# Kernel optimization log

Measured on AMD Instinct MI355X. Metric: run time of the kernel, lower is better.

Reference implementation:

```python
import jax, jax.numpy as jnp
import numpy as np

N_NODES = 50000
IN_FT = 64
OUT_FT = 64
J = 3
MAX_SCALE = 2 ** (J - 1)  # 4
TOTAL_DIM = IN_FT * (1 + (J - 1) + J * (J - 1) // 2)  # 6*IN_FT = 384
N_EDGES = 800000


def setup_inputs() -> dict:
    key = jax.random.key(0)
    k1, k2, k3, k4, k5 = jax.random.split(key, 5)
    seq = jax.random.normal(k1, (N_NODES, IN_FT), dtype=jnp.float32)
    edge_index = jax.random.randint(k2, (2, N_EDGES), 0, N_NODES, dtype=jnp.int32)
    edge_weight = jax.random.uniform(k3, (N_EDGES,), dtype=jnp.float32)
    # xavier_normal_ with gain=1.414 on fc.weight [OUT_FT, TOTAL_DIM]
    std = 1.414 * np.sqrt(2.0 / (OUT_FT + TOTAL_DIM))
    fc_w = jax.random.normal(k4, (OUT_FT, TOTAL_DIM), dtype=jnp.float32) * std
    bias = jnp.zeros((OUT_FT,), dtype=jnp.float32)
    prelu_a = jnp.array(0.25, dtype=jnp.float32)  # nn.PReLU default single param
    return {"seq": seq, "edge_index": edge_index, "edge_weight": edge_weight,
            "fc_w": fc_w, "bias": bias, "prelu_a": prelu_a}


def reference(seq, edge_index, edge_weight, fc_w, bias, prelu_a):
    n = seq.shape[0]
    f = seq.shape[1]
    src, dst = edge_index[0], edge_index[1]

    def spmm(x):  # gather source features, scale by edge weight, scatter-add to dest
        return jax.ops.segment_sum(x[src] * edge_weight[:, None], dst, num_segments=n)

    diff_list = []
    x_curr = seq
    for step in range(1, MAX_SCALE + 1):
        x_curr = spmm(x_curr)
        if step & (step - 1) == 0:
            diff_list.append(x_curr)

    F0 = diff_list[-1]
    F1 = jnp.concatenate([jnp.abs(diff_list[i - 1] - diff_list[i])
                          for i in range(1, len(diff_list))], axis=1)

    # second-order features: diffuse concatenated U, take abs diffs of blocks
    U = jnp.concatenate(diff_list, axis=1)  # [N, J*f]
    U_diff = [U]
    for _ in range(1, MAX_SCALE):
        U_diff.append(spmm(U_diff[-1]))
    feats2 = []
    for j in range(J):
        for jp in range(j + 1, J):
            s, e = j * f, (j + 1) * f
            feats2.append(jnp.abs(U_diff[jp][:, s:e] - U_diff[jp - 1][:, s:e]))
    F2 = jnp.concatenate(feats2, axis=1)

    feats = jnp.concatenate([F0, F1, F2], axis=1)  # [N, 6*f]
    out = feats @ fc_w.T + bias
    return jnp.where(out > 0, out, prelu_a * out)
```

## Files before the change

### kernel.cpp

```cpp
#include <hip/hip_runtime.h>
#include <hip/hip_bf16.h>

typedef short short8 __attribute__((ext_vector_type(8)));
typedef float f32x4 __attribute__((ext_vector_type(4)));

static constexpr int F = 64;
static constexpr int TOT = 384;
static constexpr int SLOT = 64;
static constexpr int CAP = 1536;
static constexpr int EPB = 4096;
static constexpr int WPN = 20480;

__device__ __forceinline__ unsigned short f2bf(float f) {
    unsigned u = __builtin_bit_cast(unsigned, f);
    u += 0x7fffu + ((u >> 16) & 1u);
    return (unsigned short)(u >> 16);
}
__device__ __forceinline__ float bflo(unsigned u) {
    return __builtin_bit_cast(float, u << 16);
}
__device__ __forceinline__ float bfhi(unsigned u) {
    return __builtin_bit_cast(float, u & 0xffff0000u);
}


__global__ __launch_bounds__(256) void combo_kernel(
    const float* __restrict__ x, unsigned* __restrict__ xb,
    const float* __restrict__ fcw, unsigned short* __restrict__ wp,
    int* __restrict__ gcur, long long total8, int cvtblocks, int nbuck)
{
    int b = blockIdx.x;
    if (b < cvtblocks) {
        long long i = (long long)b * 256 + threadIdx.x;
        if (i >= total8) return;
        const float4 f0 = *(const float4*)(x + i * 8);
        const float4 f1 = *(const float4*)(x + i * 8 + 4);
        uint4 o;
        o.x = (unsigned)f2bf(f0.x) | ((unsigned)f2bf(f0.y) << 16);
        o.y = (unsigned)f2bf(f0.z) | ((unsigned)f2bf(f0.w) << 16);
        o.z = (unsigned)f2bf(f1.x) | ((unsigned)f2bf(f1.y) << 16);
        o.w = (unsigned)f2bf(f1.z) | ((unsigned)f2bf(f1.w) << 16);
        *(uint4*)(xb + i * 4) = o;
    } else if (b == cvtblocks) {
        for (int e = threadIdx.x; e < WPN; e += 256) {
            int j = e & 7;
            int l = (e >> 3) & 63;
            int t = (e >> 9) & 3;
            int s = e >> 11;
            int k  = s * 32 + ((l >> 4) << 3) + j;
            int nn = t * 16 + (l & 15);
            int c  = k & 63;
            float v;
            if (k < 64)       v = fcw[nn * TOT + c];
            else if (k < 128) v = fcw[nn * TOT + 64 + c] + fcw[nn * TOT + 192 + c];
            else if (k < 192) v = fcw[nn * TOT + 128 + c];
            else if (k < 256) v = fcw[nn * TOT + 256 + c];
            else              v = fcw[nn * TOT + 320 + c];
            wp[e] = f2bf(v);
        }
    } else {
        for (int i = threadIdx.x; i < nbuck; i += 256) gcur[i] = 0;
    }
}


__global__ __launch_bounds__(256) void scatter_bucket(
    const int* __restrict__ src, const int* __restrict__ dst,
    const float* __restrict__ ew, int* __restrict__ gcur,
    int2* __restrict__ ebuf, int ne)
{
    __shared__ int hist[1024];
    __shared__ int base[1024];
    for (int i = threadIdx.x; i < 1024; i += 256) hist[i] = 0;
    __syncthreads();

    long long b0 = (long long)blockIdx.x * EPB;
    int sv[16]; int dv[16]; float wv[16];
#pragma unroll
    for (int j = 0; j < 4; ++j) {
        long long i = b0 + (long long)(threadIdx.x + 256 * j) * 4;
        if (i + 3 < ne) {
            int4   s = *(const int4*)(src + i);
            int4   d = *(const int4*)(dst + i);
            float4 w = *(const float4*)(ew + i);
            sv[j*4+0]=s.x; sv[j*4+1]=s.y; sv[j*4+2]=s.z; sv[j*4+3]=s.w;
            dv[j*4+0]=d.x; dv[j*4+1]=d.y; dv[j*4+2]=d.z; dv[j*4+3]=d.w;
            wv[j*4+0]=w.x; wv[j*4+1]=w.y; wv[j*4+2]=w.z; wv[j*4+3]=w.w;
        } else {
#pragma unroll
            for (int c = 0; c < 4; ++c) {
                long long e = i + c;
                if (e < ne) { sv[j*4+c]=src[e]; dv[j*4+c]=dst[e]; wv[j*4+c]=ew[e]; }
                else dv[j*4+c] = -1;
            }
        }
    }
#pragma unroll
    for (int c = 0; c < 16; ++c)
        if (dv[c] >= 0) atomicAdd(&hist[dv[c] >> 6], 1);
    __syncthreads();
    for (int i = threadIdx.x; i < 1024; i += 256) {
        int h = hist[i];
        base[i] = h ? atomicAdd(&gcur[i], h) : 0;
        hist[i] = 0;
    }
    __syncthreads();
#pragma unroll
    for (int c = 0; c < 16; ++c) {
        int d = dv[c];
        if (d < 0) continue;
        int b = d >> 6;
        int p = base[b] + atomicAdd(&hist[b], 1);
        if (p < CAP)
            ebuf[(long long)b * CAP + p] =
                make_int2(sv[c] | ((d & 63) << 26), __float_as_int(wv[c]));
    }
}


__global__ __launch_bounds__(256) void bucket_to_slots(
    const int2* __restrict__ ebuf, const int* __restrict__ gcur,
    int2* __restrict__ csr, int* __restrict__ cnt, int n)
{
    __shared__ int lcnt[64];
    int b = blockIdx.x;
    if (threadIdx.x < 64) lcnt[threadIdx.x] = 0;
    __syncthreads();
    int m = min(gcur[b], CAP);
    long long eb = (long long)b * CAP;
    for (int i = threadIdx.x; i < m; i += 256) {
        int2 r = ebuf[eb + i];
        int dl = (r.x >> 26) & 63;
        int s  = r.x & 0x03ffffff;
        int p  = atomicAdd(&lcnt[dl], 1);
        if (p < SLOT) {
            long long node = ((long long)b << 6) + dl;
            csr[(node << 6) + p] = make_int2(s, r.y);
        }
    }
    __syncthreads();
    if (threadIdx.x < 64) {
        int node = (b << 6) + threadIdx.x;
        if (node < n) cnt[node] = min(lcnt[threadIdx.x], SLOT);
    }
}


__global__ __launch_bounds__(256) void spmm_bf16(
    const unsigned short* __restrict__ xb, unsigned short* __restrict__ yb,
    const int* __restrict__ cnt, const int2* __restrict__ csr, int n)
{
    int wid  = (blockIdx.x * 256 + threadIdx.x) >> 6;
    int lane = threadIdx.x & 63;
    if (wid >= n) return;
    int deg = min(cnt[wid], SLOT);
    long long beg = (long long)wid << 6;
    int g  = lane >> 3;
    int fi = lane & 7;

    float a0[8], a1[8];
#pragma unroll
    for (int i = 0; i < 8; ++i) { a0[i] = 0.f; a1[i] = 0.f; }

    for (int k = 0; k < deg; k += 16) {
        int e0 = k + 2 * g, e1 = e0 + 1;
        int s0 = 0, s1 = 0;
        float w0 = 0.f, w1 = 0.f;
        if (e0 < deg) { int2 r = csr[beg + e0]; s0 = r.x; w0 = __int_as_float(r.y); }
        if (e1 < deg) { int2 r = csr[beg + e1]; s1 = r.x; w1 = __int_as_float(r.y); }
        uint4 xa = *(const uint4*)(xb + (long long)s0 * F + fi * 8);
        uint4 xc = *(const uint4*)(xb + (long long)s1 * F + fi * 8);
        a0[0] += w0 * bflo(xa.x); a0[1] += w0 * bfhi(xa.x);
        a0[2] += w0 * bflo(xa.y); a0[3] += w0 * bfhi(xa.y);
        a0[4] += w0 * bflo(xa.z); a0[5] += w0 * bfhi(xa.z);
        a0[6] += w0 * bflo(xa.w); a0[7] += w0 * bfhi(xa.w);
        a1[0] += w1 * bflo(xc.x); a1[1] += w1 * bfhi(xc.x);
        a1[2] += w1 * bflo(xc.y); a1[3] += w1 * bfhi(xc.y);
        a1[4] += w1 * bflo(xc.z); a1[5] += w1 * bfhi(xc.z);
        a1[6] += w1 * bflo(xc.w); a1[7] += w1 * bfhi(xc.w);
    }
#pragma unroll
    for (int i = 0; i < 8; ++i) a0[i] += a1[i];
#pragma unroll
    for (int m = 8; m < 64; m <<= 1) {
#pragma unroll
        for (int i = 0; i < 8; ++i) a0[i] += __shfl_xor(a0[i], m, 64);
    }
    if (lane < 8) {
        uint4 o;
        o.x = (unsigned)f2bf(a0[0]) | ((unsigned)f2bf(a0[1]) << 16);
        o.y = (unsigned)f2bf(a0[2]) | ((unsigned)f2bf(a0[3]) << 16);
        o.z = (unsigned)f2bf(a0[4]) | ((unsigned)f2bf(a0[5]) << 16);
        o.w = (unsigned)f2bf(a0[6]) | ((unsigned)f2bf(a0[7]) << 16);
        *(uint4*)(yb + (long long)wid * F + fi * 8) = o;
    }
}


__global__ __launch_bounds__(256) void gemm_mfma2(
    const unsigned short* __restrict__ y1, const unsigned short* __restrict__ y2,
    const unsigned short* __restrict__ y3, const unsigned short* __restrict__ y4,
    const unsigned short* __restrict__ wp, const float* __restrict__ bias,
    const float* __restrict__ pa, float* __restrict__ out, int n)
{
    int lane = threadIdx.x & 63;
    int wid  = (blockIdx.x * 256 + threadIdx.x) >> 6;
    int m0   = wid * 16;
    if (m0 >= n) return;

    int r  = m0 + (lane & 15);
    int cb = (lane >> 4) * 8;
    float yv0[16], yv1[16], yv2[16], yv3[16];
    {
        const unsigned short* b0 = y1 + (long long)r * F;
        const unsigned short* b1 = y2 + (long long)r * F;
        const unsigned short* b2 = y3 + (long long)r * F;
        const unsigned short* b3 = y4 + (long long)r * F;
#define LOADSEG(dstv, bp)                                                     \
        {                                                                     \
            uint4 u0 = *(const uint4*)((bp) + cb);                            \
            uint4 u1 = *(const uint4*)((bp) + 32 + cb);                       \
            dstv[0]  = bflo(u0.x); dstv[1]  = bfhi(u0.x);                     \
            dstv[2]  = bflo(u0.y); dstv[3]  = bfhi(u0.y);                     \
            dstv[4]  = bflo(u0.z); dstv[5]  = bfhi(u0.z);                     \
            dstv[6]  = bflo(u0.w); dstv[7]  = bfhi(u0.w);                     \
            dstv[8]  = bflo(u1.x); dstv[9]  = bfhi(u1.x);                     \
            dstv[10] = bflo(u1.y); dstv[11] = bfhi(u1.y);                     \
            dstv[12] = bflo(u1.z); dstv[13] = bfhi(u1.z);                     \
            dstv[14] = bflo(u1.w); dstv[15] = bfhi(u1.w);                     \
        }
        LOADSEG(yv0, b0)
        LOADSEG(yv1, b1)
        LOADSEG(yv2, b2)
        LOADSEG(yv3, b3)
#undef LOADSEG
    }

    const short8* wps = (const short8*)wp;

    f32x4 acc0 = {0.f, 0.f, 0.f, 0.f};
    f32x4 acc1 = acc0, acc2 = acc0, acc3 = acc0;

#pragma unroll
    for (int s = 0; s < 10; ++s) {
        const int fb = s >> 1;
        const int h  = s & 1;
        short8 af;
#pragma unroll
        for (int j = 0; j < 8; ++j) {
            int ci = h * 8 + j;
            float fv;
            if (fb == 0)      fv = yv3[ci];
            else if (fb == 1) fv = fabsf(yv0[ci] - yv1[ci]);
            else if (fb == 2) fv = fabsf(yv1[ci] - yv3[ci]);
            else if (fb == 3) fv = fabsf(yv2[ci] - yv1[ci]);
            else              fv = fabsf(yv3[ci] - yv2[ci]);
            af[j] = (short)f2bf(fv);
        }
        short8 bf0 = wps[(s * 4 + 0) * 64 + lane];
        short8 bf1 = wps[(s * 4 + 1) * 64 + lane];
        short8 bf2 = wps[(s * 4 + 2) * 64 + lane];
        short8 bf3 = wps[(s * 4 + 3) * 64 + lane];
        acc0 = __builtin_amdgcn_mfma_f32_16x16x32_bf16(af, bf0, acc0, 0, 0, 0);
        acc1 = __builtin_amdgcn_mfma_f32_16x16x32_bf16(af, bf1, acc1, 0, 0, 0);
        acc2 = __builtin_amdgcn_mfma_f32_16x16x32_bf16(af, bf2, acc2, 0, 0, 0);
        acc3 = __builtin_amdgcn_mfma_f32_16x16x32_bf16(af, bf3, acc3, 0, 0, 0);
    }

    float a = pa[0];
    int orow = m0 + (lane >> 4) * 4;
    int ocol = lane & 15;
#define WRITE_T(accv, t)                                                      \
    {                                                                         \
        float bco = bias[(t) * 16 + ocol];                                    \
        _Pragma("unroll")                                                     \
        for (int v = 0; v < 4; ++v) {                                         \
            float val = accv[v] + bco;                                        \
            val = val > 0.f ? val : a * val;                                  \
            out[(long long)(orow + v) * F + (t) * 16 + ocol] = val;           \
        }                                                                     \
    }
    WRITE_T(acc0, 0)
    WRITE_T(acc1, 1)
    WRITE_T(acc2, 2)
    WRITE_T(acc3, 3)
#undef WRITE_T
}

extern "C" void kernel_launch(void* const* d_in, const int* in_sizes, int n_in,
                              void* d_out, int out_size, void* d_ws, size_t ws_size,
                              hipStream_t stream)
{
    const float* seq  = (const float*)d_in[0];
    const int*   eidx = (const int*)d_in[1];
    const float* ew   = (const float*)d_in[2];
    const float* fcw  = (const float*)d_in[3];
    const float* bias = (const float*)d_in[4];
    const float* pa   = (const float*)d_in[5];
    float* out = (float*)d_out;

    int n  = in_sizes[0] / F;
    int ne = in_sizes[2];
    const int* src = eidx;
    const int* dst = eidx + ne;

    long long nF = (long long)n * F;
    int nbuck = (n + 63) >> 6;

    unsigned short* xb  = (unsigned short*)d_ws;
    unsigned short* yb1 = xb  + nF;
    unsigned short* yb2 = yb1 + nF;
    unsigned short* yb3 = yb2 + nF;
    unsigned short* yb4 = yb3 + nF;
    int2* ebuf = (int2*)yb3;
    int2* csr  = (int2*)(yb4 + nF);
    int*  cnt  = (int*)(csr + (long long)n * SLOT);
    int*  gcur = cnt + ((n + 3) & ~3);
    unsigned short* wp = (unsigned short*)(gcur + ((nbuck + 3) & ~3));

    long long total8 = nF / 8;
    int cvtblocks = (int)((total8 + 255) / 256);
    combo_kernel<<<cvtblocks + 2, 256, 0, stream>>>(
        seq, (unsigned*)xb, fcw, wp, gcur, total8, cvtblocks, nbuck);

    int bb = (ne + EPB - 1) / EPB;
    scatter_bucket<<<bb, 256, 0, stream>>>(src, dst, ew, gcur, ebuf, ne);
    bucket_to_slots<<<nbuck, 256, 0, stream>>>(ebuf, gcur, csr, cnt, n);

    int sb = (int)((nF + 255) / 256);
    spmm_bf16<<<sb, 256, 0, stream>>>(xb,  yb1, cnt, csr, n);
    spmm_bf16<<<sb, 256, 0, stream>>>(yb1, yb2, cnt, csr, n);
    spmm_bf16<<<sb, 256, 0, stream>>>(yb2, yb3, cnt, csr, n);
    spmm_bf16<<<sb, 256, 0, stream>>>(yb3, yb4, cnt, csr, n);

    int gw = (n + 15) / 16;
    int gb = (gw * 64 + 255) / 256;
    gemm_mfma2<<<gb, 256, 0, stream>>>(yb1, yb2, yb3, yb4, wp, bias, pa, out, n);
}
```

Baseline: 152.0 us.

## Split bf16 feature arrays into two 32-wide halves for cache-friendlier SpMM gathers

Node features and diffusion outputs are stored as two separate half arrays of 32 bf16 each, instead of one 64-wide array. The SpMM kernel now launches twice as many waves: the first n waves process the low half and the rest process the high half, each gathering 64-byte rows with 16 edges per iteration. The aim is to halve the random-gather working set per pass so it fits better in the L2 cache. The cost is reading the CSR edge list twice and doing more shuffle-reduction steps. The conversion and GEMM kernels are adapted to the split layout.

Result: slower. 204.7 us (+34.7%).

```diff
diff --git a/kernel.cpp b/kernel.cpp
--- a/kernel.cpp
+++ b/kernel.cpp
@@ -5,6 +5,7 @@
 typedef float f32x4 __attribute__((ext_vector_type(4)));
 
 static constexpr int F = 64;
+static constexpr int H = 32;
 static constexpr int TOT = 384;
 static constexpr int SLOT = 64;
 static constexpr int CAP = 1536;
@@ -25,7 +26,8 @@
 
 
 __global__ __launch_bounds__(256) void combo_kernel(
-    const float* __restrict__ x, unsigned* __restrict__ xb,
+    const float* __restrict__ x, unsigned short* __restrict__ xbl,
+    unsigned short* __restrict__ xbh,
     const float* __restrict__ fcw, unsigned short* __restrict__ wp,
     int* __restrict__ gcur, long long total8, int cvtblocks, int nbuck)
 {
@@ -40,7 +42,10 @@
         o.y = (unsigned)f2bf(f0.z) | ((unsigned)f2bf(f0.w) << 16);
         o.z = (unsigned)f2bf(f1.x) | ((unsigned)f2bf(f1.y) << 16);
         o.w = (unsigned)f2bf(f1.z) | ((unsigned)f2bf(f1.w) << 16);
-        *(uint4*)(xb + i * 4) = o;
+        long long node = i >> 3;
+        int seg = (int)(i & 7);
+        unsigned short* dstb = (seg < 4) ? xbl : xbh;
+        *(uint4*)(dstb + node * H + (seg & 3) * 8) = o;
     } else if (b == cvtblocks) {
         for (int e = threadIdx.x; e < WPN; e += 256) {
             int j = e & 7;
@@ -146,60 +151,58 @@
 }
 
 
-__global__ __launch_bounds__(256) void spmm_bf16(
-    const unsigned short* __restrict__ xb, unsigned short* __restrict__ yb,
+__global__ __launch_bounds__(256) void spmm_half(
+    const unsigned short* __restrict__ xl, const unsigned short* __restrict__ xh,
+    unsigned short* __restrict__ yl, unsigned short* __restrict__ yh,
     const int* __restrict__ cnt, const int2* __restrict__ csr, int n)
 {
-    int wid  = (blockIdx.x * 256 + threadIdx.x) >> 6;
+    int wid2 = (blockIdx.x * 256 + threadIdx.x) >> 6;
     int lane = threadIdx.x & 63;
-    if (wid >= n) return;
-    int deg = min(cnt[wid], SLOT);
-    long long beg = (long long)wid << 6;
-    int g  = lane >> 3;
-    int fi = lane & 7;
-
-    float a0[8], a1[8];
-#pragma unroll
-    for (int i = 0; i < 8; ++i) { a0[i] = 0.f; a1[i] = 0.f; }
+    int node = wid2;
+    const unsigned short* xp = xl;
+    unsigned short* yp = yl;
+    if (wid2 >= n) { node = wid2 - n; xp = xh; yp = yh; }
+    if (node >= n) return;
+    int deg = min(cnt[node], SLOT);
+    long long beg = (long long)node << 6;
+    int g  = lane >> 2;
+    int fi = lane & 3;
+
+    float a[8];
+#pragma unroll
+    for (int i = 0; i < 8; ++i) a[i] = 0.f;
 
     for (int k = 0; k < deg; k += 16) {
-        int e0 = k + 2 * g, e1 = e0 + 1;
-        int s0 = 0, s1 = 0;
-        float w0 = 0.f, w1 = 0.f;
-        if (e0 < deg) { int2 r = csr[beg + e0]; s0 = r.x; w0 = __int_as_float(r.y); }
-        if (e1 < deg) { int2 r = csr[beg + e1]; s1 = r.x; w1 = __int_as_float(r.y); }
-        uint4 xa = *(const uint4*)(xb + (long long)s0 * F + fi * 8);
-        uint4 xc = *(const uint4*)(xb + (long long)s1 * F + fi * 8);
-        a0[0] += w0 * bflo(xa.x); a0[1] += w0 * bfhi(xa.x);
-        a0[2] += w0 * bflo(xa.y); a0[3] += w0 * bfhi(xa.y);
-        a0[4] += w0 * bflo(xa.z); a0[5] += w0 * bfhi(xa.z);
-        a0[6] += w0 * bflo(xa.w); a0[7] += w0 * bfhi(xa.w);
-        a1[0] += w1 * bflo(xc.x); a1[1] += w1 * bfhi(xc.x);
-        a1[2] += w1 * bflo(xc.y); a1[3] += w1 * bfhi(xc.y);
-        a1[4] += w1 * bflo(xc.z); a1[5] += w1 * bfhi(xc.z);
-        a1[6] += w1 * bflo(xc.w); a1[7] += w1 * bfhi(xc.w);
-    }
-#pragma unroll
-    for (int i = 0; i < 8; ++i) a0[i] += a1[i];
-#pragma unroll
-    for (int m = 8; m < 64; m <<= 1) {
-#pragma unroll
-        for (int i = 0; i < 8; ++i) a0[i] += __shfl_xor(a0[i], m, 64);
-    }
-    if (lane < 8) {
+        int e = k + g;
+        int s = 0; float w = 0.f;
+        if (e < deg) { int2 r = csr[beg + e]; s = r.x; w = __int_as_float(r.y); }
+        uint4 xv = *(const uint4*)(xp + (long long)s * H + fi * 8);
+        a[0] += w * bflo(xv.x); a[1] += w * bfhi(xv.x);
+        a[2] += w * bflo(xv.y); a[3] += w * bfhi(xv.y);
+        a[4] += w * bflo(xv.z); a[5] += w * bfhi(xv.z);
+        a[6] += w * bflo(xv.w); a[7] += w * bfhi(xv.w);
+    }
+#pragma unroll
+    for (int m = 4; m < 64; m <<= 1) {
+#pragma unroll
+        for (int i = 0; i < 8; ++i) a[i] += __shfl_xor(a[i], m, 64);
+    }
+    if (lane < 4) {
         uint4 o;
-        o.x = (unsigned)f2bf(a0[0]) | ((unsigned)f2bf(a0[1]) << 16);
-        o.y = (unsigned)f2bf(a0[2]) | ((unsigned)f2bf(a0[3]) << 16);
-        o.z = (unsigned)f2bf(a0[4]) | ((unsigned)f2bf(a0[5]) << 16);
-        o.w = (unsigned)f2bf(a0[6]) | ((unsigned)f2bf(a0[7]) << 16);
-        *(uint4*)(yb + (long long)wid * F + fi * 8) = o;
+        o.x = (unsigned)f2bf(a[0]) | ((unsigned)f2bf(a[1]) << 16);
+        o.y = (unsigned)f2bf(a[2]) | ((unsigned)f2bf(a[3]) << 16);
+        o.z = (unsigned)f2bf(a[4]) | ((unsigned)f2bf(a[5]) << 16);
+        o.w = (unsigned)f2bf(a[6]) | ((unsigned)f2bf(a[7]) << 16);
+        *(uint4*)(yp + (long long)node * H + fi * 8) = o;
     }
 }
 
 
 __global__ __launch_bounds__(256) void gemm_mfma2(
-    const unsigned short* __restrict__ y1, const unsigned short* __restrict__ y2,
-    const unsigned short* __restrict__ y3, const unsigned short* __restrict__ y4,
+    const unsigned short* __restrict__ y1l, const unsigned short* __restrict__ y1h,
+    const unsigned short* __restrict__ y2l, const unsigned short* __restrict__ y2h,
+    const unsigned short* __restrict__ y3l, const unsigned short* __restrict__ y3h,
+    const unsigned short* __restrict__ y4l, const unsigned short* __restrict__ y4h,
     const unsigned short* __restrict__ wp, const float* __restrict__ bias,
     const float* __restrict__ pa, float* __restrict__ out, int n)
 {
@@ -208,18 +211,14 @@
     int m0   = wid * 16;
     if (m0 >= n) return;
 
-    int r  = m0 + (lane & 15);
+    long long r = m0 + (lane & 15);
     int cb = (lane >> 4) * 8;
     float yv0[16], yv1[16], yv2[16], yv3[16];
     {
-        const unsigned short* b0 = y1 + (long long)r * F;
-        const unsigned short* b1 = y2 + (long long)r * F;
-        const unsigned short* b2 = y3 + (long long)r * F;
-        const unsigned short* b3 = y4 + (long long)r * F;
-#define LOADSEG(dstv, bp)                                                     \
+#define LOADSEG2(dstv, lo, hi)                                                \
         {                                                                     \
-            uint4 u0 = *(const uint4*)((bp) + cb);                            \
-            uint4 u1 = *(const uint4*)((bp) + 32 + cb);                       \
+            uint4 u0 = *(const uint4*)((lo) + r * H + cb);                    \
+            uint4 u1 = *(const uint4*)((hi) + r * H + cb);                    \
             dstv[0]  = bflo(u0.x); dstv[1]  = bfhi(u0.x);                     \
             dstv[2]  = bflo(u0.y); dstv[3]  = bfhi(u0.y);                     \
             dstv[4]  = bflo(u0.z); dstv[5]  = bfhi(u0.z);                     \
@@ -229,11 +228,11 @@
             dstv[12] = bflo(u1.z); dstv[13] = bfhi(u1.z);                     \
             dstv[14] = bflo(u1.w); dstv[15] = bfhi(u1.w);                     \
         }
-        LOADSEG(yv0, b0)
-        LOADSEG(yv1, b1)
-        LOADSEG(yv2, b2)
-        LOADSEG(yv3, b3)
-#undef LOADSEG
+        LOADSEG2(yv0, y1l, y1h)
+        LOADSEG2(yv1, y2l, y2h)
+        LOADSEG2(yv2, y3l, y3h)
+        LOADSEG2(yv3, y4l, y4h)
+#undef LOADSEG2
     }
 
     const short8* wps = (const short8*)wp;
@@ -304,36 +303,42 @@
     const int* src = eidx;
     const int* dst = eidx + ne;
 
-    long long nF = (long long)n * F;
+    long long hn = (long long)n * H;
     int nbuck = (n + 63) >> 6;
 
-    unsigned short* xb  = (unsigned short*)d_ws;
-    unsigned short* yb1 = xb  + nF;
-    unsigned short* yb2 = yb1 + nF;
-    unsigned short* yb3 = yb2 + nF;
-    unsigned short* yb4 = yb3 + nF;
-    int2* ebuf = (int2*)yb3;
-    int2* csr  = (int2*)(yb4 + nF);
+    unsigned short* xbl = (unsigned short*)d_ws;
+    unsigned short* xbh = xbl + hn;
+    unsigned short* y1l = xbh + hn;
+    unsigned short* y1h = y1l + hn;
+    unsigned short* y2l = y1h + hn;
+    unsigned short* y2h = y2l + hn;
+    unsigned short* y3l = y2h + hn;
+    unsigned short* y3h = y3l + hn;
+    unsigned short* y4l = y3h + hn;
+    unsigned short* y4h = y4l + hn;
+    int2* ebuf = (int2*)y1l;
+    int2* csr  = (int2*)(y4h + hn);
     int*  cnt  = (int*)(csr + (long long)n * SLOT);
     int*  gcur = cnt + ((n + 3) & ~3);
     unsigned short* wp = (unsigned short*)(gcur + ((nbuck + 3) & ~3));
 
-    long long total8 = nF / 8;
+    long long total8 = (long long)n * 8;
     int cvtblocks = (int)((total8 + 255) / 256);
     combo_kernel<<<cvtblocks + 2, 256, 0, stream>>>(
-        seq, (unsigned*)xb, fcw, wp, gcur, total8, cvtblocks, nbuck);
+        seq, xbl, xbh, fcw, wp, gcur, total8, cvtblocks, nbuck);
 
     int bb = (ne + EPB - 1) / EPB;
     scatter_bucket<<<bb, 256, 0, stream>>>(src, dst, ew, gcur, ebuf, ne);
     bucket_to_slots<<<nbuck, 256, 0, stream>>>(ebuf, gcur, csr, cnt, n);
 
-    int sb = (int)((nF + 255) / 256);
-    spmm_bf16<<<sb, 256, 0, stream>>>(xb,  yb1, cnt, csr, n);
-    spmm_bf16<<<sb, 256, 0, stream>>>(yb1, yb2, cnt, csr, n);
-    spmm_bf16<<<sb, 256, 0, stream>>>(yb2, yb3, cnt, csr, n);
-    spmm_bf16<<<sb, 256, 0, stream>>>(yb3, yb4, cnt, csr, n);
+    int sb2 = (int)(((long long)2 * n * 64 + 255) / 256);
+    spmm_half<<<sb2, 256, 0, stream>>>(xbl, xbh, y1l, y1h, cnt, csr, n);
+    spmm_half<<<sb2, 256, 0, stream>>>(y1l, y1h, y2l, y2h, cnt, csr, n);
+    spmm_half<<<sb2, 256, 0, stream>>>(y2l, y2h, y3l, y3h, cnt, csr, n);
+    spmm_half<<<sb2, 256, 0, stream>>>(y3l, y3h, y4l, y4h, cnt, csr, n);
 
     int gw = (n + 15) / 16;
     int gb = (gw * 64 + 255) / 256;
-    gemm_mfma2<<<gb, 256, 0, stream>>>(yb1, yb2, yb3, yb4, wp, bias, pa, out, n);
-}
+    gemm_mfma2<<<gb, 256, 0, stream>>>(y1l, y1h, y2l, y2h, y3l, y3h, y4l, y4h,
+                                       wp, bias, pa, out, n);
+}
```
